# Optimization experiments

Measured on AMD Instinct MI355X. Metric: run time of the kernel, lower is better.

## Reference

```python
import jax, jax.numpy as jnp
import numpy as np

B, N, M, G, F = 8, 1000, 64, 50, 128


def setup_inputs() -> dict:
    key = jax.random.key(0)
    ks = jax.random.split(key, 9)
    s = 0.05
    return {
        "features": jax.random.normal(ks[0], (B, N, F), jnp.float32),
        "rbf_expansion": jax.random.uniform(ks[1], (B, N, M, G), jnp.float32),
        "neighbor_list": jax.random.randint(ks[2], (B, N, M), 0, N, jnp.int64),
        "W_init": jax.random.normal(ks[3], (F, F), jnp.float32) * s,
        "W1": jax.random.normal(ks[4], (G, F), jnp.float32) * s,
        "b1": jnp.zeros((F,), jnp.float32),
        "W2": jax.random.normal(ks[5], (F, F), jnp.float32) * s,
        "b2": jnp.zeros((F,), jnp.float32),
        "nbr_w": jax.random.normal(ks[6], (F,), jnp.float32) * s,
        "Wo1": jax.random.normal(ks[7], (F, F), jnp.float32) * s,
        "bo1": jnp.zeros((F,), jnp.float32),
        "Wo2": jax.random.normal(ks[8], (F, F), jnp.float32) * s,
        "bo2": jnp.zeros((F,), jnp.float32),
    }


def reference(features, rbf_expansion, neighbor_list, W_init, W1, b1, W2, b2,
              nbr_w, Wo1, bo1, Wo2, bo2):
    b, n, m = neighbor_list.shape
    # 1. atom-wise linear, no bias/activation: [B,N,F]
    init = features @ W_init
    # 2. CFConv: filter generator on RBF expansion -> [B,N,M,F]
    filt = jnp.tanh(rbf_expansion @ W1 + b1) @ W2 + b2
    # gather neighbor features: init[b, neighbor_list[b,n,m], :] -> [B,N,M,F]
    idx = neighbor_list.reshape(b, n * m, 1)
    nbr_feat = jnp.take_along_axis(init, idx, axis=1).reshape(b, n, m, -1)
    conv = nbr_feat * filt
    # attention over neighbors via learned vector nbr_w
    attn = jax.nn.softmax(jnp.einsum('bnmf,f->bnm', conv, nbr_w), axis=-1)
    agg = jnp.einsum('bnm,bnmf->bnf', attn, conv)
    # 3-4. output dense: linear+tanh, then linear
    out = jnp.tanh(agg @ Wo1 + bo1) @ Wo2 + bo2
    return out, attn
```

## Files before the change

kernel.cpp:

```cpp
#include <hip/hip_runtime.h>
#include <hip/hip_bf16.h>

typedef __attribute__((ext_vector_type(8))) short short8;
typedef __attribute__((ext_vector_type(4))) float f32x4;
typedef unsigned short u16;
typedef unsigned int u32;

#define NBATCH 8
#define NA 1000
#define MD 64
#define GD 50
#define FD 128
#define TOTAL (NBATCH * NA)

__device__ __forceinline__ u16 f2bf(float f) {
    u32 x = __float_as_uint(f);
    return (u16)((x + 0x7fffu + ((x >> 16) & 1u)) >> 16);
}
__device__ __forceinline__ float bf2f(u16 u) {
    return __uint_as_float(((u32)u) << 16);
}
__device__ __forceinline__ u32 pkbf(float x, float y) {
    __hip_bfloat162 h = __float22bfloat162_rn(float2{x, y});
    return *reinterpret_cast<u32*>(&h);
}
__device__ __forceinline__ float tanh_fast(float x) {
    float e = __expf(2.0f * x);
    return 1.0f - 2.0f * __builtin_amdgcn_rcpf(e + 1.0f);
}
__device__ __forceinline__ f32x4 mfma16(short8 a, short8 b, f32x4 c) {
    return __builtin_amdgcn_mfma_f32_16x16x32_bf16(a, b, c, 0, 0, 0);
}

__global__ void k0_prep(const float* __restrict__ W1, const float* __restrict__ W2,
                        const float* __restrict__ Wi, const float* __restrict__ Wo1,
                        const float* __restrict__ Wo2,
                        u16* __restrict__ W1P, u16* __restrict__ W2P,
                        u16* __restrict__ WiP, u16* __restrict__ Wo1P,
                        u16* __restrict__ Wo2P) {
    const int g0 = blockIdx.x * 256 + threadIdx.x;
    const int gstep = gridDim.x * 256;
    for (int p = g0; p < 16 * 512; p += gstep) {
        int seg = p >> 9, l = (p >> 3) & 63, j = p & 7;
        int ks = seg >> 3, nt = seg & 7;
        int k = ks * 32 + ((l >> 4) << 3) + j;
        int n = nt * 16 + (l & 15);
        W1P[p] = (k < GD) ? f2bf(W1[k * FD + n]) : (u16)0;
    }
    for (int p = g0; p < 32 * 512; p += gstep) {
        int seg = p >> 9, l = (p >> 3) & 63, j = p & 7;
        int half = seg >> 4, ks = (seg >> 3) & 1, nt = seg & 7;
        int k = half * 64 + ks * 32 + ((l >> 4) << 3) + j;
        int n = nt * 16 + (l & 15);
        int idx = k * FD + n;
        W2P[p]  = f2bf(W2[idx]);
        WiP[p]  = f2bf(Wi[idx]);
        Wo1P[p] = f2bf(Wo1[idx]);
        Wo2P[p] = f2bf(Wo2[idx]);
    }
}

__global__ __launch_bounds__(64) void k1_init(const float* __restrict__ feat,
                                              const u16* __restrict__ WiP,
                                              u16* __restrict__ initB) {
    const int lane = threadIdx.x;
    const int quad = lane >> 4, col = lane & 15;
    const int row0 = blockIdx.x * 16;

    f32x4 acc[8];
    const f32x4 zf = {0.f, 0.f, 0.f, 0.f};
#pragma unroll
    for (int nt = 0; nt < 8; ++nt) acc[nt] = zf;

#pragma unroll
    for (int half = 0; half < 2; ++half)
#pragma unroll
        for (int ks = 0; ks < 2; ++ks) {
            const int ka = half * 64 + ks * 32 + quad * 8;
            const float* src = &feat[(size_t)(row0 + col) * FD + ka];
            float4 v0 = *(const float4*)src;
            float4 v1 = *(const float4*)(src + 4);
            short8 a;
            u32* ap = (u32*)&a;
            ap[0] = pkbf(v0.x, v0.y);
            ap[1] = pkbf(v0.z, v0.w);
            ap[2] = pkbf(v1.x, v1.y);
            ap[3] = pkbf(v1.z, v1.w);
#pragma unroll
            for (int nt = 0; nt < 8; ++nt) {
                short8 bfr = *(const short8*)&WiP[(((half * 2 + ks) * 8 + nt) << 9) + (lane << 3)];
                acc[nt] = mfma16(a, bfr, acc[nt]);
            }
        }
#pragma unroll
    for (int nt = 0; nt < 8; ++nt)
#pragma unroll
        for (int r = 0; r < 4; ++r)
            initB[(size_t)(row0 + quad * 4 + r) * FD + nt * 16 + col] = f2bf(acc[nt][r]);
}

__global__ __launch_bounds__(256, 4) void k2_main(
    const float* __restrict__ rbf, const int* __restrict__ nl,
    const u16* __restrict__ initB,
    const u16* __restrict__ W1P, const u16* __restrict__ W2P,
    const float* __restrict__ b1, const float* __restrict__ b2,
    const float* __restrict__ nbrw,
    float* __restrict__ aggOut, float* __restrict__ attnO) {
    __shared__ alignas(16) char smem[34816];
    const int tid = threadIdx.x, wid = tid >> 6, lane = tid & 63;
    const int quad = lane >> 4, col = lane & 15, rw = wid * 32;
    const int blk = blockIdx.x;
    const int b = blk / 500;
    const int n0 = (blk - b * 500) * 2;
    const int atom0 = b * NA + n0;

    u16* wv = (u16*)smem + wid * 4352;
    float* logitS = (float*)smem;
    float* aggS   = (float*)(smem + 1024);

    int rowoff[2][4];
#pragma unroll
    for (int mt = 0; mt < 2; ++mt)
#pragma unroll
        for (int r = 0; r < 4; ++r)
            rowoff[mt][r] = (b * NA + nl[atom0 * MD + rw + mt * 16 + quad * 4 + r]) * FD;

    {
        const float* rsrc = rbf + (size_t)(atom0 * MD + rw) * GD;
        for (int i = lane; i < 800; i += 64) {
            int e = 2 * i;
            int r = e / 50, g = e - r * 50;
            float2 v = *(const float2*)&rsrc[e];
            *(u32*)&wv[r * 68 + g] = pkbf(v.x, v.y);
        }
        for (int i = lane; i < 448; i += 64) {
            int r = i / 14;
            wv[r * 68 + 50 + (i - r * 14)] = 0;
        }
    }

    f32x4 acc[2][8];
    const f32x4 zf = {0.f, 0.f, 0.f, 0.f};
#pragma unroll
    for (int mt = 0; mt < 2; ++mt)
#pragma unroll
        for (int nt = 0; nt < 8; ++nt) acc[mt][nt] = zf;
#pragma unroll
    for (int ks = 0; ks < 2; ++ks) {
        const int ka = ks * 32 + quad * 8;
        short8 a0 = *(const short8*)&wv[col * 68 + ka];
        short8 a1 = *(const short8*)&wv[(16 + col) * 68 + ka];
#pragma unroll
        for (int nt = 0; nt < 8; ++nt) {
            short8 bfr = *(const short8*)&W1P[((ks * 8 + nt) << 9) + (lane << 3)];
            acc[0][nt] = mfma16(a0, bfr, acc[0][nt]);
            acc[1][nt] = mfma16(a1, bfr, acc[1][nt]);
        }
    }

    float bias[8];
#pragma unroll
    for (int nt = 0; nt < 8; ++nt) bias[nt] = b1[nt * 16 + col];
#pragma unroll
    for (int mt = 0; mt < 2; ++mt)
#pragma unroll
        for (int nt = 0; nt < 8; ++nt)
#pragma unroll
            for (int r = 0; r < 4; ++r) {
                int row = mt * 16 + quad * 4 + r;
                wv[row * 136 + nt * 16 + col] =
                    f2bf(tanh_fast(acc[mt][nt][r] + bias[nt]));
            }

    f32x4 acc2[2][8];
#pragma unroll
    for (int mt = 0; mt < 2; ++mt)
#pragma unroll
        for (int nt = 0; nt < 8; ++nt) acc2[mt][nt] = zf;
#pragma unroll
    for (int half = 0; half < 2; ++half)
#pragma unroll
        for (int ks = 0; ks < 2; ++ks) {
            const int ka = half * 64 + ks * 32 + quad * 8;
            short8 a0 = *(const short8*)&wv[col * 136 + ka];
            short8 a1 = *(const short8*)&wv[(16 + col) * 136 + ka];
#pragma unroll
            for (int nt = 0; nt < 8; ++nt) {
                short8 bfr = *(const short8*)&W2P[(((half * 2 + ks) * 8 + nt) << 9) + (lane << 3)];
                acc2[0][nt] = mfma16(a0, bfr, acc2[0][nt]);
                acc2[1][nt] = mfma16(a1, bfr, acc2[1][nt]);
            }
        }

    float wv8[8];
#pragma unroll
    for (int nt = 0; nt < 8; ++nt) {
        bias[nt] = b2[nt * 16 + col];
        wv8[nt] = nbrw[nt * 16 + col];
    }
    float part[2][4] = {{0.f, 0.f, 0.f, 0.f}, {0.f, 0.f, 0.f, 0.f}};
#pragma unroll
    for (int mt = 0; mt < 2; ++mt)
#pragma unroll
        for (int nt = 0; nt < 8; ++nt)
#pragma unroll
            for (int r = 0; r < 4; ++r) {
                float nb = bf2f(initB[rowoff[mt][r] + nt * 16 + col]);
                float cv = nb * (acc2[mt][nt][r] + bias[nt]);
                acc2[mt][nt][r] = cv;
                part[mt][r] += cv * wv8[nt];
            }
#pragma unroll
    for (int d = 1; d < 16; d <<= 1)
#pragma unroll
        for (int mt = 0; mt < 2; ++mt)
#pragma unroll
            for (int r = 0; r < 4; ++r)
                part[mt][r] += __shfl_xor(part[mt][r], d, 64);

    __syncthreads();
    if (col == 0) {
#pragma unroll
        for (int mt = 0; mt < 2; ++mt)
#pragma unroll
            for (int r = 0; r < 4; ++r)
                logitS[rw + mt * 16 + quad * 4 + r] = part[mt][r];
    }
    __syncthreads();

    float attw[2][4];
    {
        const int base = rw & 64;
        float x = logitS[base + lane];
        float m = x;
#pragma unroll
        for (int d = 1; d < 64; d <<= 1) m = fmaxf(m, __shfl_xor(m, d, 64));
        float e = __expf(x - m);
        float s = e;
#pragma unroll
        for (int d = 1; d < 64; d <<= 1) s += __shfl_xor(s, d, 64);
        float a = e / s;
        if ((wid & 1) == 0)
            attnO[(size_t)(atom0 + (wid >> 1)) * MD + lane] = a;
#pragma unroll
        for (int mt = 0; mt < 2; ++mt)
#pragma unroll
            for (int r = 0; r < 4; ++r)
                attw[mt][r] = __shfl(a, (rw & 32) + mt * 16 + quad * 4 + r, 64);
    }

    float aggp[8] = {0.f, 0.f, 0.f, 0.f, 0.f, 0.f, 0.f, 0.f};
#pragma unroll
    for (int mt = 0; mt < 2; ++mt)
#pragma unroll
        for (int r = 0; r < 4; ++r) {
            float a = attw[mt][r];
#pragma unroll
            for (int nt = 0; nt < 8; ++nt) aggp[nt] += a * acc2[mt][nt][r];
        }
#pragma unroll
    for (int d = 16; d < 64; d <<= 1)
#pragma unroll
        for (int nt = 0; nt < 8; ++nt) aggp[nt] += __shfl_xor(aggp[nt], d, 64);
    if (quad == 0) {
#pragma unroll
        for (int nt = 0; nt < 8; ++nt) aggS[wid * 128 + nt * 16 + col] = aggp[nt];
    }
    __syncthreads();
    {
        int a = tid >> 7;
        int c = tid & 127;
        float v = aggS[(2 * a) * 128 + c] + aggS[(2 * a + 1) * 128 + c];
        aggOut[(size_t)(atom0 + a) * FD + c] = v;
    }
}

__global__ __launch_bounds__(64) void k3_out(
    float* __restrict__ outp, const u16* __restrict__ Wo1P,
    const u16* __restrict__ Wo2P, const float* __restrict__ bo1,
    const float* __restrict__ bo2) {
    __shared__ alignas(16) u16 sT[16 * 136];
    const int lane = threadIdx.x;
    const int quad = lane >> 4, col = lane & 15;
    const int row0 = blockIdx.x * 16;

    f32x4 acc[8];
    const f32x4 zf = {0.f, 0.f, 0.f, 0.f};
#pragma unroll
    for (int nt = 0; nt < 8; ++nt) acc[nt] = zf;
#pragma unroll
    for (int half = 0; half < 2; ++half)
#pragma unroll
        for (int ks = 0; ks < 2; ++ks) {
            const int ka = half * 64 + ks * 32 + quad * 8;
            const float* src = &outp[(size_t)(row0 + col) * FD + ka];
            float4 v0 = *(const float4*)src;
            float4 v1 = *(const float4*)(src + 4);
            short8 a;
            u32* ap = (u32*)&a;
            ap[0] = pkbf(v0.x, v0.y);
            ap[1] = pkbf(v0.z, v0.w);
            ap[2] = pkbf(v1.x, v1.y);
            ap[3] = pkbf(v1.z, v1.w);
#pragma unroll
            for (int nt = 0; nt < 8; ++nt) {
                short8 bfr = *(const short8*)&Wo1P[(((half * 2 + ks) * 8 + nt) << 9) + (lane << 3)];
                acc[nt] = mfma16(a, bfr, acc[nt]);
            }
        }

#pragma unroll
    for (int nt = 0; nt < 8; ++nt) {
        float bias = bo1[nt * 16 + col];
#pragma unroll
        for (int r = 0; r < 4; ++r)
            sT[(quad * 4 + r) * 136 + nt * 16 + col] =
                f2bf(tanh_fast(acc[nt][r] + bias));
    }
    __syncthreads();

    f32x4 acc2[8];
#pragma unroll
    for (int nt = 0; nt < 8; ++nt) acc2[nt] = zf;
#pragma unroll
    for (int half = 0; half < 2; ++half)
#pragma unroll
        for (int ks = 0; ks < 2; ++ks) {
            const int ka = half * 64 + ks * 32 + quad * 8;
            short8 a0 = *(const short8*)&sT[col * 136 + ka];
#pragma unroll
            for (int nt = 0; nt < 8; ++nt) {
                short8 bfr = *(const short8*)&Wo2P[(((half * 2 + ks) * 8 + nt) << 9) + (lane << 3)];
                acc2[nt] = mfma16(a0, bfr, acc2[nt]);
            }
        }
#pragma unroll
    for (int nt = 0; nt < 8; ++nt) {
        float bias = bo2[nt * 16 + col];
#pragma unroll
        for (int r = 0; r < 4; ++r)
            outp[(size_t)(row0 + quad * 4 + r) * FD + nt * 16 + col] =
                acc2[nt][r] + bias;
    }
}

extern "C" void kernel_launch(void* const* d_in, const int* in_sizes, int n_in,
                              void* d_out, int out_size, void* d_ws,
                              size_t ws_size, hipStream_t stream) {
    const float* feat = (const float*)d_in[0];
    const float* rbf  = (const float*)d_in[1];
    const int*   nl   = (const int*)d_in[2];
    const float* Wi   = (const float*)d_in[3];
    const float* W1   = (const float*)d_in[4];
    const float* b1   = (const float*)d_in[5];
    const float* W2   = (const float*)d_in[6];
    const float* b2   = (const float*)d_in[7];
    const float* nbrw = (const float*)d_in[8];
    const float* Wo1  = (const float*)d_in[9];
    const float* bo1  = (const float*)d_in[10];
    const float* Wo2  = (const float*)d_in[11];
    const float* bo2  = (const float*)d_in[12];

    float* outp  = (float*)d_out;
    float* attnp = outp + (size_t)TOTAL * FD;

    char* ws = (char*)d_ws;
    u16* initB = (u16*)ws;
    u16* W1P   = (u16*)(ws + 2048000);
    u16* W2P   = (u16*)(ws + 2064384);
    u16* WiP   = (u16*)(ws + 2097152);
    u16* Wo1P  = (u16*)(ws + 2129920);
    u16* Wo2P  = (u16*)(ws + 2162688);

    hipLaunchKernelGGL(k0_prep, dim3(40), dim3(256), 0, stream,
                       W1, W2, Wi, Wo1, Wo2, W1P, W2P, WiP, Wo1P, Wo2P);
    hipLaunchKernelGGL(k1_init, dim3(500), dim3(64), 0, stream, feat, WiP, initB);
    hipLaunchKernelGGL(k2_main, dim3(4000), dim3(256), 0, stream,
                       rbf, nl, initB, W1P, W2P, b1, b2, nbrw, outp, attnp);
    hipLaunchKernelGGL(k3_out, dim3(500), dim3(64), 0, stream,
                       outp, Wo1P, Wo2P, bo1, bo2);
}
```

Baseline: 261.2 us.

## Fuse four kernels into one persistent cooperative kernel with grid syncs

Replaces the four separate launches (weight prep, init linear, main CFConv/attention, output MLP) with one cooperative persistent kernel. The phases are separated by grid-wide syncs, and blocks loop over work items in a grid-stride fashion. This removes the launch and inter-kernel gaps. In exchange it adds three grid barriers, and the small phases now run with fewer, larger blocks (a wave per 16-row tile), which may reduce parallelism compared with 500 separate blocks.

```diff
diff --git a/kernel.cpp b/kernel.cpp
--- a/kernel.cpp
+++ b/kernel.cpp
@@ -1,5 +1,8 @@
 #include <hip/hip_runtime.h>
 #include <hip/hip_bf16.h>
+#include <hip/hip_cooperative_groups.h>
+
+namespace cg = cooperative_groups;
 
 typedef __attribute__((ext_vector_type(8))) short short8;
 typedef __attribute__((ext_vector_type(4))) float f32x4;
@@ -32,14 +35,25 @@
     return __builtin_amdgcn_mfma_f32_16x16x32_bf16(a, b, c, 0, 0, 0);
 }
 
-__global__ void k0_prep(const float* __restrict__ W1, const float* __restrict__ W2,
-                        const float* __restrict__ Wi, const float* __restrict__ Wo1,
-                        const float* __restrict__ Wo2,
-                        u16* __restrict__ W1P, u16* __restrict__ W2P,
-                        u16* __restrict__ WiP, u16* __restrict__ Wo1P,
-                        u16* __restrict__ Wo2P) {
-    const int g0 = blockIdx.x * 256 + threadIdx.x;
-    const int gstep = gridDim.x * 256;
+__global__ __launch_bounds__(256, 4) void fused(
+    const float* __restrict__ feat, const float* __restrict__ rbf,
+    const int* __restrict__ nl,
+    const float* __restrict__ Wi, const float* __restrict__ W1,
+    const float* __restrict__ b1, const float* __restrict__ W2,
+    const float* __restrict__ b2, const float* __restrict__ nbrw,
+    const float* __restrict__ Wo1, const float* __restrict__ bo1,
+    const float* __restrict__ Wo2, const float* __restrict__ bo2,
+    u16* __restrict__ initB, u16* __restrict__ W1P, u16* __restrict__ W2P,
+    u16* __restrict__ WiP, u16* __restrict__ Wo1P, u16* __restrict__ Wo2P,
+    float* __restrict__ outp, float* __restrict__ attnp) {
+    cg::grid_group grid = cg::this_grid();
+    __shared__ alignas(16) char smem[34816];
+    const int tid = threadIdx.x, wid = tid >> 6, lane = tid & 63;
+    const int quad = lane >> 4, col = lane & 15, rw = wid * 32;
+    const int nblk = gridDim.x, blk = blockIdx.x;
+    const int g0 = blk * 256 + tid, gstep = nblk * 256;
+    const f32x4 zf = {0.f, 0.f, 0.f, 0.f};
+
     for (int p = g0; p < 16 * 512; p += gstep) {
         int seg = p >> 9, l = (p >> 3) & 63, j = p & 7;
         int ks = seg >> 3, nt = seg & 7;
@@ -58,289 +72,272 @@
         Wo1P[p] = f2bf(Wo1[idx]);
         Wo2P[p] = f2bf(Wo2[idx]);
     }
-}
-
-__global__ __launch_bounds__(64) void k1_init(const float* __restrict__ feat,
-                                              const u16* __restrict__ WiP,
-                                              u16* __restrict__ initB) {
-    const int lane = threadIdx.x;
-    const int quad = lane >> 4, col = lane & 15;
-    const int row0 = blockIdx.x * 16;
-
-    f32x4 acc[8];
-    const f32x4 zf = {0.f, 0.f, 0.f, 0.f};
-#pragma unroll
-    for (int nt = 0; nt < 8; ++nt) acc[nt] = zf;
-
-#pragma unroll
-    for (int half = 0; half < 2; ++half)
-#pragma unroll
-        for (int ks = 0; ks < 2; ++ks) {
-            const int ka = half * 64 + ks * 32 + quad * 8;
-            const float* src = &feat[(size_t)(row0 + col) * FD + ka];
-            float4 v0 = *(const float4*)src;
-            float4 v1 = *(const float4*)(src + 4);
-            short8 a;
-            u32* ap = (u32*)&a;
-            ap[0] = pkbf(v0.x, v0.y);
-            ap[1] = pkbf(v0.z, v0.w);
-            ap[2] = pkbf(v1.x, v1.y);
-            ap[3] = pkbf(v1.z, v1.w);
-#pragma unroll
-            for (int nt = 0; nt < 8; ++nt) {
-                short8 bfr = *(const short8*)&WiP[(((half * 2 + ks) * 8 + nt) << 9) + (lane << 3)];
-                acc[nt] = mfma16(a, bfr, acc[nt]);
-            }
+    __threadfence();
+    grid.sync();
+
+    for (int t = blk * 4 + wid; t < 500; t += nblk * 4) {
+        const int row0 = t * 16;
+        f32x4 acc[8];
+#pragma unroll
+        for (int nt = 0; nt < 8; ++nt) acc[nt] = zf;
+#pragma unroll
+        for (int half = 0; half < 2; ++half)
+#pragma unroll
+            for (int ks = 0; ks < 2; ++ks) {
+                const int ka = half * 64 + ks * 32 + quad * 8;
+                const float* src = &feat[(size_t)(row0 + col) * FD + ka];
+                float4 v0 = *(const float4*)src;
+                float4 v1 = *(const float4*)(src + 4);
+                short8 a;
+                u32* ap = (u32*)&a;
+                ap[0] = pkbf(v0.x, v0.y);
+                ap[1] = pkbf(v0.z, v0.w);
+                ap[2] = pkbf(v1.x, v1.y);
+                ap[3] = pkbf(v1.z, v1.w);
+#pragma unroll
+                for (int nt = 0; nt < 8; ++nt) {
+                    short8 bfr = *(const short8*)&WiP[(((half * 2 + ks) * 8 + nt) << 9) + (lane << 3)];
+                    acc[nt] = mfma16(a, bfr, acc[nt]);
+                }
+            }
+#pragma unroll
+        for (int nt = 0; nt < 8; ++nt)
+#pragma unroll
+            for (int r = 0; r < 4; ++r)
+                initB[(size_t)(row0 + quad * 4 + r) * FD + nt * 16 + col] = f2bf(acc[nt][r]);
+    }
+    __threadfence();
+    grid.sync();
+
+    {
+        u16* wv = (u16*)smem + wid * 4352;
+        float* logitS = (float*)smem;
+        float* aggS   = (float*)(smem + 1024);
+
+        float b1v[8], b2v[8], wvv[8];
+#pragma unroll
+        for (int nt = 0; nt < 8; ++nt) {
+            b1v[nt] = b1[nt * 16 + col];
+            b2v[nt] = b2[nt * 16 + col];
+            wvv[nt] = nbrw[nt * 16 + col];
         }
-#pragma unroll
-    for (int nt = 0; nt < 8; ++nt)
-#pragma unroll
-        for (int r = 0; r < 4; ++r)
-            initB[(size_t)(row0 + quad * 4 + r) * FD + nt * 16 + col] = f2bf(acc[nt][r]);
-}
-
-__global__ __launch_bounds__(256, 4) void k2_main(
-    const float* __restrict__ rbf, const int* __restrict__ nl,
-    const u16* __restrict__ initB,
-    const u16* __restrict__ W1P, const u16* __restrict__ W2P,
-    const float* __restrict__ b1, const float* __restrict__ b2,
-    const float* __restrict__ nbrw,
-    float* __restrict__ aggOut, float* __restrict__ attnO) {
-    __shared__ alignas(16) char smem[34816];
-    const int tid = threadIdx.x, wid = tid >> 6, lane = tid & 63;
-    const int quad = lane >> 4, col = lane & 15, rw = wid * 32;
-    const int blk = blockIdx.x;
-    const int b = blk / 500;
-    const int n0 = (blk - b * 500) * 2;
-    const int atom0 = b * NA + n0;
-
-    u16* wv = (u16*)smem + wid * 4352;
-    float* logitS = (float*)smem;
-    float* aggS   = (float*)(smem + 1024);
-
-    int rowoff[2][4];
-#pragma unroll
-    for (int mt = 0; mt < 2; ++mt)
-#pragma unroll
-        for (int r = 0; r < 4; ++r)
-            rowoff[mt][r] = (b * NA + nl[atom0 * MD + rw + mt * 16 + quad * 4 + r]) * FD;
-
-    {
-        const float* rsrc = rbf + (size_t)(atom0 * MD + rw) * GD;
-        for (int i = lane; i < 800; i += 64) {
-            int e = 2 * i;
-            int r = e / 50, g = e - r * 50;
-            float2 v = *(const float2*)&rsrc[e];
-            *(u32*)&wv[r * 68 + g] = pkbf(v.x, v.y);
+
+        for (int pair = blk; pair < 4000; pair += nblk) {
+            const int b = pair / 500;
+            const int n0 = (pair - b * 500) * 2;
+            const int atom0 = b * NA + n0;
+
+            int rowoff[2][4];
+#pragma unroll
+            for (int mt = 0; mt < 2; ++mt)
+#pragma unroll
+                for (int r = 0; r < 4; ++r)
+                    rowoff[mt][r] = (b * NA + nl[atom0 * MD + rw + mt * 16 + quad * 4 + r]) * FD;
+
+            {
+                const float* rsrc = rbf + (size_t)(atom0 * MD + rw) * GD;
+                for (int i = lane; i < 800; i += 64) {
+                    int e = 2 * i;
+                    int r = e / 50, g = e - r * 50;
+                    float2 v = *(const float2*)&rsrc[e];
+                    *(u32*)&wv[r * 68 + g] = pkbf(v.x, v.y);
+                }
+                for (int i = lane; i < 448; i += 64) {
+                    int r = i / 14;
+                    wv[r * 68 + 50 + (i - r * 14)] = 0;
+                }
+            }
+
+            f32x4 acc[2][8];
+#pragma unroll
+            for (int mt = 0; mt < 2; ++mt)
+#pragma unroll
+                for (int nt = 0; nt < 8; ++nt) acc[mt][nt] = zf;
+#pragma unroll
+            for (int ks = 0; ks < 2; ++ks) {
+                const int ka = ks * 32 + quad * 8;
+                short8 a0 = *(const short8*)&wv[col * 68 + ka];
+                short8 a1 = *(const short8*)&wv[(16 + col) * 68 + ka];
+#pragma unroll
+                for (int nt = 0; nt < 8; ++nt) {
+                    short8 bfr = *(const short8*)&W1P[((ks * 8 + nt) << 9) + (lane << 3)];
+                    acc[0][nt] = mfma16(a0, bfr, acc[0][nt]);
+                    acc[1][nt] = mfma16(a1, bfr, acc[1][nt]);
+                }
+            }
+
+#pragma unroll
+            for (int mt = 0; mt < 2; ++mt)
+#pragma unroll
+                for (int nt = 0; nt < 8; ++nt)
+#pragma unroll
+                    for (int r = 0; r < 4; ++r) {
+                        int row = mt * 16 + quad * 4 + r;
+                        wv[row * 136 + nt * 16 + col] =
+                            f2bf(tanh_fast(acc[mt][nt][r] + b1v[nt]));
+                    }
+
+            f32x4 acc2[2][8];
+#pragma unroll
+            for (int mt = 0; mt < 2; ++mt)
+#pragma unroll
+                for (int nt = 0; nt < 8; ++nt) acc2[mt][nt] = zf;
+#pragma unroll
+            for (int half = 0; half < 2; ++half)
+#pragma unroll
+                for (int ks = 0; ks < 2; ++ks) {
+                    const int ka = half * 64 + ks * 32 + quad * 8;
+                    short8 a0 = *(const short8*)&wv[col * 136 + ka];
+                    short8 a1 = *(const short8*)&wv[(16 + col) * 136 + ka];
+#pragma unroll
+                    for (int nt = 0; nt < 8; ++nt) {
+                        short8 bfr = *(const short8*)&W2P[(((half * 2 + ks) * 8 + nt) << 9) + (lane << 3)];
+                        acc2[0][nt] = mfma16(a0, bfr, acc2[0][nt]);
+                        acc2[1][nt] = mfma16(a1, bfr, acc2[1][nt]);
+                    }
+                }
+
+            float part[2][4] = {{0.f, 0.f, 0.f, 0.f}, {0.f, 0.f, 0.f, 0.f}};
+#pragma unroll
+            for (int mt = 0; mt < 2; ++mt)
+#pragma unroll
+                for (int nt = 0; nt < 8; ++nt)
+#pragma unroll
+                    for (int r = 0; r < 4; ++r) {
+                        float nb = bf2f(initB[rowoff[mt][r] + nt * 16 + col]);
+                        float cv = nb * (acc2[mt][nt][r] + b2v[nt]);
+                        acc2[mt][nt][r] = cv;
+                        part[mt][r] += cv * wvv[nt];
+                    }
+#pragma unroll
+            for (int d = 1; d < 16; d <<= 1)
+#pragma unroll
+                for (int mt = 0; mt < 2; ++mt)
+#pragma unroll
+                    for (int r = 0; r < 4; ++r)
+                        part[mt][r] += __shfl_xor(part[mt][r], d, 64);
+
+            __syncthreads();
+            if (col == 0) {
+#pragma unroll
+                for (int mt = 0; mt < 2; ++mt)
+#pragma unroll
+                    for (int r = 0; r < 4; ++r)
+                        logitS[rw + mt * 16 + quad * 4 + r] = part[mt][r];
+            }
+            __syncthreads();
+
+            float attw[2][4];
+            {
+                const int base = rw & 64;
+                float x = logitS[base + lane];
+                float m = x;
+#pragma unroll
+                for (int d = 1; d < 64; d <<= 1) m = fmaxf(m, __shfl_xor(m, d, 64));
+                float e = __expf(x - m);
+                float s = e;
+#pragma unroll
+                for (int d = 1; d < 64; d <<= 1) s += __shfl_xor(s, d, 64);
+                float a = e / s;
+                if ((wid & 1) == 0)
+                    attnp[(size_t)(atom0 + (wid >> 1)) * MD + lane] = a;
+#pragma unroll
+                for (int mt = 0; mt < 2; ++mt)
+#pragma unroll
+                    for (int r = 0; r < 4; ++r)
+                        attw[mt][r] = __shfl(a, (rw & 32) + mt * 16 + quad * 4 + r, 64);
+            }
+
+            float aggp[8] = {0.f, 0.f, 0.f, 0.f, 0.f, 0.f, 0.f, 0.f};
+#pragma unroll
+            for (int mt = 0; mt < 2; ++mt)
+#pragma unroll
+                for (int r = 0; r < 4; ++r) {
+                    float a = attw[mt][r];
+#pragma unroll
+                    for (int nt = 0; nt < 8; ++nt) aggp[nt] += a * acc2[mt][nt][r];
+                }
+#pragma unroll
+            for (int d = 16; d < 64; d <<= 1)
+#pragma unroll
+                for (int nt = 0; nt < 8; ++nt) aggp[nt] += __shfl_xor(aggp[nt], d, 64);
+            if (quad == 0) {
+#pragma unroll
+                for (int nt = 0; nt < 8; ++nt) aggS[wid * 128 + nt * 16 + col] = aggp[nt];
+            }
+            __syncthreads();
+            {
+                int a = tid >> 7;
+                int c = tid & 127;
+                float v = aggS[(2 * a) * 128 + c] + aggS[(2 * a + 1) * 128 + c];
+                outp[(size_t)(atom0 + a) * FD + c] = v;
+            }
+            __syncthreads();
         }
-        for (int i = lane; i < 448; i += 64) {
-            int r = i / 14;
-            wv[r * 68 + 50 + (i - r * 14)] = 0;
+    }
+    __threadfence();
+    grid.sync();
+
+    for (int t = blk * 4 + wid; t < 500; t += nblk * 4) {
+        const int row0 = t * 16;
+        u16* sT = (u16*)(smem + wid * 8704);
+
+        f32x4 acc[8];
+#pragma unroll
+        for (int nt = 0; nt < 8; ++nt) acc[nt] = zf;
+#pragma unroll
+        for (int half = 0; half < 2; ++half)
+#pragma unroll
+            for (int ks = 0; ks < 2; ++ks) {
+                const int ka = half * 64 + ks * 32 + quad * 8;
+                const float* src = &outp[(size_t)(row0 + col) * FD + ka];
+                float4 v0 = *(const float4*)src;
+                float4 v1 = *(const float4*)(src + 4);
+                short8 a;
+                u32* ap = (u32*)&a;
+                ap[0] = pkbf(v0.x, v0.y);
+                ap[1] = pkbf(v0.z, v0.w);
+                ap[2] = pkbf(v1.x, v1.y);
+                ap[3] = pkbf(v1.z, v1.w);
+#pragma unroll
+                for (int nt = 0; nt < 8; ++nt) {
+                    short8 bfr = *(const short8*)&Wo1P[(((half * 2 + ks) * 8 + nt) << 9) + (lane << 3)];
+                    acc[nt] = mfma16(a, bfr, acc[nt]);
+                }
+            }
+
+#pragma unroll
+        for (int nt = 0; nt < 8; ++nt) {
+            float bias = bo1[nt * 16 + col];
+#pragma unroll
+            for (int r = 0; r < 4; ++r)
+                sT[(quad * 4 + r) * 136 + nt * 16 + col] =
+                    f2bf(tanh_fast(acc[nt][r] + bias));
         }
-    }
-
-    f32x4 acc[2][8];
-    const f32x4 zf = {0.f, 0.f, 0.f, 0.f};
-#pragma unroll
-    for (int mt = 0; mt < 2; ++mt)
-#pragma unroll
-        for (int nt = 0; nt < 8; ++nt) acc[mt][nt] = zf;
-#pragma unroll
-    for (int ks = 0; ks < 2; ++ks) {
-        const int ka = ks * 32 + quad * 8;
-        short8 a0 = *(const short8*)&wv[col * 68 + ka];
-        short8 a1 = *(const short8*)&wv[(16 + col) * 68 + ka];
+
+        f32x4 acc2[8];
+#pragma unroll
+        for (int nt = 0; nt < 8; ++nt) acc2[nt] = zf;
+#pragma unroll
+        for (int half = 0; half < 2; ++half)
+#pragma unroll
+            for (int ks = 0; ks < 2; ++ks) {
+                const int ka = half * 64 + ks * 32 + quad * 8;
+                short8 a0 = *(const short8*)&sT[col * 136 + ka];
+#pragma unroll
+                for (int nt = 0; nt < 8; ++nt) {
+                    short8 bfr = *(const short8*)&Wo2P[(((half * 2 + ks) * 8 + nt) << 9) + (lane << 3)];
+                    acc2[nt] = mfma16(a0, bfr, acc2[nt]);
+                }
+            }
 #pragma unroll
         for (int nt = 0; nt < 8; ++nt) {
-            short8 bfr = *(const short8*)&W1P[((ks * 8 + nt) << 9) + (lane << 3)];
-            acc[0][nt] = mfma16(a0, bfr, acc[0][nt]);
-            acc[1][nt] = mfma16(a1, bfr, acc[1][nt]);
+            float bias = bo2[nt * 16 + col];
+#pragma unroll
+            for (int r = 0; r < 4; ++r)
+                outp[(size_t)(row0 + quad * 4 + r) * FD + nt * 16 + col] =
+                    acc2[nt][r] + bias;
         }
-    }
-
-    float bias[8];
-#pragma unroll
-    for (int nt = 0; nt < 8; ++nt) bias[nt] = b1[nt * 16 + col];
-#pragma unroll
-    for (int mt = 0; mt < 2; ++mt)
-#pragma unroll
-        for (int nt = 0; nt < 8; ++nt)
-#pragma unroll
-            for (int r = 0; r < 4; ++r) {
-                int row = mt * 16 + quad * 4 + r;
-                wv[row * 136 + nt * 16 + col] =
-                    f2bf(tanh_fast(acc[mt][nt][r] + bias[nt]));
-            }
-
-    f32x4 acc2[2][8];
-#pragma unroll
-    for (int mt = 0; mt < 2; ++mt)
-#pragma unroll
-        for (int nt = 0; nt < 8; ++nt) acc2[mt][nt] = zf;
-#pragma unroll
-    for (int half = 0; half < 2; ++half)
-#pragma unroll
-        for (int ks = 0; ks < 2; ++ks) {
-            const int ka = half * 64 + ks * 32 + quad * 8;
-            short8 a0 = *(const short8*)&wv[col * 136 + ka];
-            short8 a1 = *(const short8*)&wv[(16 + col) * 136 + ka];
-#pragma unroll
-            for (int nt = 0; nt < 8; ++nt) {
-                short8 bfr = *(const short8*)&W2P[(((half * 2 + ks) * 8 + nt) << 9) + (lane << 3)];
-                acc2[0][nt] = mfma16(a0, bfr, acc2[0][nt]);
-                acc2[1][nt] = mfma16(a1, bfr, acc2[1][nt]);
-            }
-        }
-
-    float wv8[8];
-#pragma unroll
-    for (int nt = 0; nt < 8; ++nt) {
-        bias[nt] = b2[nt * 16 + col];
-        wv8[nt] = nbrw[nt * 16 + col];
-    }
-    float part[2][4] = {{0.f, 0.f, 0.f, 0.f}, {0.f, 0.f, 0.f, 0.f}};
-#pragma unroll
-    for (int mt = 0; mt < 2; ++mt)
-#pragma unroll
-        for (int nt = 0; nt < 8; ++nt)
-#pragma unroll
-            for (int r = 0; r < 4; ++r) {
-                float nb = bf2f(initB[rowoff[mt][r] + nt * 16 + col]);
-                float cv = nb * (acc2[mt][nt][r] + bias[nt]);
-                acc2[mt][nt][r] = cv;
-                part[mt][r] += cv * wv8[nt];
-            }
-#pragma unroll
-    for (int d = 1; d < 16; d <<= 1)
-#pragma unroll
-        for (int mt = 0; mt < 2; ++mt)
-#pragma unroll
-            for (int r = 0; r < 4; ++r)
-                part[mt][r] += __shfl_xor(part[mt][r], d, 64);
-
-    __syncthreads();
-    if (col == 0) {
-#pragma unroll
-        for (int mt = 0; mt < 2; ++mt)
-#pragma unroll
-            for (int r = 0; r < 4; ++r)
-                logitS[rw + mt * 16 + quad * 4 + r] = part[mt][r];
-    }
-    __syncthreads();
-
-    float attw[2][4];
-    {
-        const int base = rw & 64;
-        float x = logitS[base + lane];
-        float m = x;
-#pragma unroll
-        for (int d = 1; d < 64; d <<= 1) m = fmaxf(m, __shfl_xor(m, d, 64));
-        float e = __expf(x - m);
-        float s = e;
-#pragma unroll
-        for (int d = 1; d < 64; d <<= 1) s += __shfl_xor(s, d, 64);
-        float a = e / s;
-        if ((wid & 1) == 0)
-            attnO[(size_t)(atom0 + (wid >> 1)) * MD + lane] = a;
-#pragma unroll
-        for (int mt = 0; mt < 2; ++mt)
-#pragma unroll
-            for (int r = 0; r < 4; ++r)
-                attw[mt][r] = __shfl(a, (rw & 32) + mt * 16 + quad * 4 + r, 64);
-    }
-
-    float aggp[8] = {0.f, 0.f, 0.f, 0.f, 0.f, 0.f, 0.f, 0.f};
-#pragma unroll
-    for (int mt = 0; mt < 2; ++mt)
-#pragma unroll
-        for (int r = 0; r < 4; ++r) {
-            float a = attw[mt][r];
-#pragma unroll
-            for (int nt = 0; nt < 8; ++nt) aggp[nt] += a * acc2[mt][nt][r];
-        }
-#pragma unroll
-    for (int d = 16; d < 64; d <<= 1)
-#pragma unroll
-        for (int nt = 0; nt < 8; ++nt) aggp[nt] += __shfl_xor(aggp[nt], d, 64);
-    if (quad == 0) {
-#pragma unroll
-        for (int nt = 0; nt < 8; ++nt) aggS[wid * 128 + nt * 16 + col] = aggp[nt];
-    }
-    __syncthreads();
-    {
-        int a = tid >> 7;
-        int c = tid & 127;
-        float v = aggS[(2 * a) * 128 + c] + aggS[(2 * a + 1) * 128 + c];
-        aggOut[(size_t)(atom0 + a) * FD + c] = v;
-    }
-}
-
-__global__ __launch_bounds__(64) void k3_out(
-    float* __restrict__ outp, const u16* __restrict__ Wo1P,
-    const u16* __restrict__ Wo2P, const float* __restrict__ bo1,
-    const float* __restrict__ bo2) {
-    __shared__ alignas(16) u16 sT[16 * 136];
-    const int lane = threadIdx.x;
-    const int quad = lane >> 4, col = lane & 15;
-    const int row0 = blockIdx.x * 16;
-
-    f32x4 acc[8];
-    const f32x4 zf = {0.f, 0.f, 0.f, 0.f};
-#pragma unroll
-    for (int nt = 0; nt < 8; ++nt) acc[nt] = zf;
-#pragma unroll
-    for (int half = 0; half < 2; ++half)
-#pragma unroll
-        for (int ks = 0; ks < 2; ++ks) {
-            const int ka = half * 64 + ks * 32 + quad * 8;
-            const float* src = &outp[(size_t)(row0 + col) * FD + ka];
-            float4 v0 = *(const float4*)src;
-            float4 v1 = *(const float4*)(src + 4);
-            short8 a;
-            u32* ap = (u32*)&a;
-            ap[0] = pkbf(v0.x, v0.y);
-            ap[1] = pkbf(v0.z, v0.w);
-            ap[2] = pkbf(v1.x, v1.y);
-            ap[3] = pkbf(v1.z, v1.w);
-#pragma unroll
-            for (int nt = 0; nt < 8; ++nt) {
-                short8 bfr = *(const short8*)&Wo1P[(((half * 2 + ks) * 8 + nt) << 9) + (lane << 3)];
-                acc[nt] = mfma16(a, bfr, acc[nt]);
-            }
-        }
-
-#pragma unroll
-    for (int nt = 0; nt < 8; ++nt) {
-        float bias = bo1[nt * 16 + col];
-#pragma unroll
-        for (int r = 0; r < 4; ++r)
-            sT[(quad * 4 + r) * 136 + nt * 16 + col] =
-                f2bf(tanh_fast(acc[nt][r] + bias));
-    }
-    __syncthreads();
-
-    f32x4 acc2[8];
-#pragma unroll
-    for (int nt = 0; nt < 8; ++nt) acc2[nt] = zf;
-#pragma unroll
-    for (int half = 0; half < 2; ++half)
-#pragma unroll
-        for (int ks = 0; ks < 2; ++ks) {
-            const int ka = half * 64 + ks * 32 + quad * 8;
-            short8 a0 = *(const short8*)&sT[col * 136 + ka];
-#pragma unroll
-            for (int nt = 0; nt < 8; ++nt) {
-                short8 bfr = *(const short8*)&Wo2P[(((half * 2 + ks) * 8 + nt) << 9) + (lane << 3)];
-                acc2[nt] = mfma16(a0, bfr, acc2[nt]);
-            }
-        }
-#pragma unroll
-    for (int nt = 0; nt < 8; ++nt) {
-        float bias = bo2[nt * 16 + col];
-#pragma unroll
-        for (int r = 0; r < 4; ++r)
-            outp[(size_t)(row0 + quad * 4 + r) * FD + nt * 16 + col] =
-                acc2[nt][r] + bias;
     }
 }
 
@@ -372,11 +369,23 @@
     u16* Wo1P  = (u16*)(ws + 2129920);
     u16* Wo2P  = (u16*)(ws + 2162688);
 
-    hipLaunchKernelGGL(k0_prep, dim3(40), dim3(256), 0, stream,
-                       W1, W2, Wi, Wo1, Wo2, W1P, W2P, WiP, Wo1P, Wo2P);
-    hipLaunchKernelGGL(k1_init, dim3(500), dim3(64), 0, stream, feat, WiP, initB);
-    hipLaunchKernelGGL(k2_main, dim3(4000), dim3(256), 0, stream,
-                       rbf, nl, initB, W1P, W2P, b1, b2, nbrw, outp, attnp);
-    hipLaunchKernelGGL(k3_out, dim3(500), dim3(64), 0, stream,
-                       outp, Wo1P, Wo2P, bo1, bo2);
-}
+    static int nblk = 0;
+    if (nblk == 0) {
+        int dev = 0;
+        hipGetDevice(&dev);
+        hipDeviceProp_t props;
+        hipGetDeviceProperties(&props, dev);
+        int mbp = 0;
+        hipOccupancyMaxActiveBlocksPerMultiprocessor(&mbp, (const void*)fused, 256, 0);
+        if (mbp < 1) mbp = 1;
+        if (mbp > 4) mbp = 4;
+        nblk = props.multiProcessorCount * mbp;
+        if (nblk > 4000) nblk = 4000;
+        if (nblk < 64) nblk = 64;
+    }
+
+    void* args[] = {&feat, &rbf, &nl, &Wi, &W1, &b1, &W2, &b2, &nbrw,
+                    &Wo1, &bo1, &Wo2, &bo2,
+                    &initB, &W1P, &W2P, &WiP, &Wo1P, &Wo2P, &outp, &attnp};
+    hipLaunchCooperativeKernel((const void*)fused, dim3(nblk), dim3(256), args, 0, stream);
+}
```

Result: slower. 847.1 us (+224.3%).

## Interleave init feature layout for vector gathers and fuse output MLP into main kernel

Applied to the files above, without the earlier changes.

Stores the bf16 init features in an interleaved column order so each neighbor row gather in the main kernel becomes one 16-byte load per lane instead of eight scalar loads. Also fuses the output dense layers into the main kernel, computing the two-atom output MLP with MFMA from shared memory, which removes a separate launch and the global round trip of the aggregated features. The fused MLP uses MFMA tiles that are mostly padding and adds extra barriers per block.

```diff
diff --git a/kernel.cpp b/kernel.cpp
--- a/kernel.cpp
+++ b/kernel.cpp
@@ -93,10 +93,12 @@
             }
         }
 #pragma unroll
-    for (int nt = 0; nt < 8; ++nt)
-#pragma unroll
-        for (int r = 0; r < 4; ++r)
-            initB[(size_t)(row0 + quad * 4 + r) * FD + nt * 16 + col] = f2bf(acc[nt][r]);
+    for (int r = 0; r < 4; ++r) {
+        short8 g;
+#pragma unroll
+        for (int nt = 0; nt < 8; ++nt) g[nt] = (short)f2bf(acc[nt][r]);
+        *(short8*)&initB[(size_t)(row0 + quad * 4 + r) * FD + col * 8] = g;
+    }
 }
 
 __global__ __launch_bounds__(256, 4) void k2_main(
@@ -105,7 +107,9 @@
     const u16* __restrict__ W1P, const u16* __restrict__ W2P,
     const float* __restrict__ b1, const float* __restrict__ b2,
     const float* __restrict__ nbrw,
-    float* __restrict__ aggOut, float* __restrict__ attnO) {
+    const u16* __restrict__ Wo1P, const u16* __restrict__ Wo2P,
+    const float* __restrict__ bo1, const float* __restrict__ bo2,
+    float* __restrict__ outp, float* __restrict__ attnO) {
     __shared__ alignas(16) char smem[34816];
     const int tid = threadIdx.x, wid = tid >> 6, lane = tid & 63;
     const int quad = lane >> 4, col = lane & 15, rw = wid * 32;
@@ -117,6 +121,8 @@
     u16* wv = (u16*)smem + wid * 4352;
     float* logitS = (float*)smem;
     float* aggS   = (float*)(smem + 1024);
+    u16* aggF = (u16*)(smem + 4096);
+    u16* t1F  = (u16*)(smem + 8704 + 4352);
 
     int rowoff[2][4];
 #pragma unroll
@@ -202,14 +208,16 @@
 #pragma unroll
     for (int mt = 0; mt < 2; ++mt)
 #pragma unroll
-        for (int nt = 0; nt < 8; ++nt)
-#pragma unroll
-            for (int r = 0; r < 4; ++r) {
-                float nb = bf2f(initB[rowoff[mt][r] + nt * 16 + col]);
+        for (int r = 0; r < 4; ++r) {
+            short8 g = *(const short8*)&initB[rowoff[mt][r] + col * 8];
+#pragma unroll
+            for (int nt = 0; nt < 8; ++nt) {
+                float nb = bf2f((u16)g[nt]);
                 float cv = nb * (acc2[mt][nt][r] + bias[nt]);
                 acc2[mt][nt][r] = cv;
                 part[mt][r] += cv * wv8[nt];
             }
+        }
 #pragma unroll
     for (int d = 1; d < 16; d <<= 1)
 #pragma unroll
@@ -267,80 +275,57 @@
         for (int nt = 0; nt < 8; ++nt) aggS[wid * 128 + nt * 16 + col] = aggp[nt];
     }
     __syncthreads();
+
     {
-        int a = tid >> 7;
-        int c = tid & 127;
+        int a = tid >> 7, c = tid & 127;
         float v = aggS[(2 * a) * 128 + c] + aggS[(2 * a + 1) * 128 + c];
-        aggOut[(size_t)(atom0 + a) * FD + c] = v;
-    }
-}
-
-__global__ __launch_bounds__(64) void k3_out(
-    float* __restrict__ outp, const u16* __restrict__ Wo1P,
-    const u16* __restrict__ Wo2P, const float* __restrict__ bo1,
-    const float* __restrict__ bo2) {
-    __shared__ alignas(16) u16 sT[16 * 136];
-    const int lane = threadIdx.x;
-    const int quad = lane >> 4, col = lane & 15;
-    const int row0 = blockIdx.x * 16;
-
-    f32x4 acc[8];
-    const f32x4 zf = {0.f, 0.f, 0.f, 0.f};
-#pragma unroll
-    for (int nt = 0; nt < 8; ++nt) acc[nt] = zf;
+        aggF[a * 136 + c] = f2bf(v);
+    }
+    __syncthreads();
+
+    f32x4 o0 = zf, o1v = zf;
 #pragma unroll
     for (int half = 0; half < 2; ++half)
 #pragma unroll
         for (int ks = 0; ks < 2; ++ks) {
             const int ka = half * 64 + ks * 32 + quad * 8;
-            const float* src = &outp[(size_t)(row0 + col) * FD + ka];
-            float4 v0 = *(const float4*)src;
-            float4 v1 = *(const float4*)(src + 4);
-            short8 a;
-            u32* ap = (u32*)&a;
-            ap[0] = pkbf(v0.x, v0.y);
-            ap[1] = pkbf(v0.z, v0.w);
-            ap[2] = pkbf(v1.x, v1.y);
-            ap[3] = pkbf(v1.z, v1.w);
-#pragma unroll
-            for (int nt = 0; nt < 8; ++nt) {
-                short8 bfr = *(const short8*)&Wo1P[(((half * 2 + ks) * 8 + nt) << 9) + (lane << 3)];
-                acc[nt] = mfma16(a, bfr, acc[nt]);
-            }
-        }
-
-#pragma unroll
-    for (int nt = 0; nt < 8; ++nt) {
-        float bias = bo1[nt * 16 + col];
-#pragma unroll
-        for (int r = 0; r < 4; ++r)
-            sT[(quad * 4 + r) * 136 + nt * 16 + col] =
-                f2bf(tanh_fast(acc[nt][r] + bias));
-    }
-    __syncthreads();
-
-    f32x4 acc2[8];
-#pragma unroll
-    for (int nt = 0; nt < 8; ++nt) acc2[nt] = zf;
+            short8 a0 = *(const short8*)&aggF[col * 136 + ka];
+            short8 bf0 = *(const short8*)&Wo1P[(((half * 2 + ks) * 8 + 2 * wid) << 9) + (lane << 3)];
+            short8 bf1 = *(const short8*)&Wo1P[(((half * 2 + ks) * 8 + 2 * wid + 1) << 9) + (lane << 3)];
+            o0 = mfma16(a0, bf0, o0);
+            o1v = mfma16(a0, bf1, o1v);
+        }
+    if (quad == 0) {
+        float bb0 = bo1[(2 * wid) * 16 + col];
+        float bb1 = bo1[(2 * wid + 1) * 16 + col];
+#pragma unroll
+        for (int r = 0; r < 2; ++r) {
+            t1F[r * 136 + (2 * wid) * 16 + col] = f2bf(tanh_fast(o0[r] + bb0));
+            t1F[r * 136 + (2 * wid + 1) * 16 + col] = f2bf(tanh_fast(o1v[r] + bb1));
+        }
+    }
+    __syncthreads();
+
+    o0 = zf; o1v = zf;
 #pragma unroll
     for (int half = 0; half < 2; ++half)
 #pragma unroll
         for (int ks = 0; ks < 2; ++ks) {
             const int ka = half * 64 + ks * 32 + quad * 8;
-            short8 a0 = *(const short8*)&sT[col * 136 + ka];
-#pragma unroll
-            for (int nt = 0; nt < 8; ++nt) {
-                short8 bfr = *(const short8*)&Wo2P[(((half * 2 + ks) * 8 + nt) << 9) + (lane << 3)];
-                acc2[nt] = mfma16(a0, bfr, acc2[nt]);
-            }
-        }
-#pragma unroll
-    for (int nt = 0; nt < 8; ++nt) {
-        float bias = bo2[nt * 16 + col];
-#pragma unroll
-        for (int r = 0; r < 4; ++r)
-            outp[(size_t)(row0 + quad * 4 + r) * FD + nt * 16 + col] =
-                acc2[nt][r] + bias;
+            short8 a0 = *(const short8*)&t1F[col * 136 + ka];
+            short8 bf0 = *(const short8*)&Wo2P[(((half * 2 + ks) * 8 + 2 * wid) << 9) + (lane << 3)];
+            short8 bf1 = *(const short8*)&Wo2P[(((half * 2 + ks) * 8 + 2 * wid + 1) << 9) + (lane << 3)];
+            o0 = mfma16(a0, bf0, o0);
+            o1v = mfma16(a0, bf1, o1v);
+        }
+    if (quad == 0) {
+        float bb0 = bo2[(2 * wid) * 16 + col];
+        float bb1 = bo2[(2 * wid + 1) * 16 + col];
+#pragma unroll
+        for (int r = 0; r < 2; ++r) {
+            outp[(size_t)(atom0 + r) * FD + (2 * wid) * 16 + col] = o0[r] + bb0;
+            outp[(size_t)(atom0 + r) * FD + (2 * wid + 1) * 16 + col] = o1v[r] + bb1;
+        }
     }
 }
 
@@ -376,7 +361,6 @@
                        W1, W2, Wi, Wo1, Wo2, W1P, W2P, WiP, Wo1P, Wo2P);
     hipLaunchKernelGGL(k1_init, dim3(500), dim3(64), 0, stream, feat, WiP, initB);
     hipLaunchKernelGGL(k2_main, dim3(4000), dim3(256), 0, stream,
-                       rbf, nl, initB, W1P, W2P, b1, b2, nbrw, outp, attnp);
-    hipLaunchKernelGGL(k3_out, dim3(500), dim3(64), 0, stream,
-                       outp, Wo1P, Wo2P, bo1, bo2);
-}
+                       rbf, nl, initB, W1P, W2P, b1, b2, nbrw,
+                       Wo1P, Wo2P, bo1, bo2, outp, attnp);
+}
```

Measured after the change: 268.1 us. +2.6%, slower.

## Permute feature layout for vectorized bf16 stores and gathers; fold biases into accumulators

Applied to the files above, without the earlier changes.

Stores the init features and intermediate tanh activations in a column-permuted order, so each lane writes and reads one 16-byte short8 instead of eight scattered 2-byte elements. W2 and Wo2 get matching K-permuted packing so the GEMMs still compute the right result. The main win sought is vectorising the random neighbor gather from initB in k2. Biases are also preloaded into the MFMA accumulators, which removes the separate add. This adds coupling between the prep permutation and the consumer kernels, so any mismatch would silently corrupt results.

```diff
diff --git a/kernel.cpp b/kernel.cpp
--- a/kernel.cpp
+++ b/kernel.cpp
@@ -50,13 +50,13 @@
     for (int p = g0; p < 32 * 512; p += gstep) {
         int seg = p >> 9, l = (p >> 3) & 63, j = p & 7;
         int half = seg >> 4, ks = (seg >> 3) & 1, nt = seg & 7;
-        int k = half * 64 + ks * 32 + ((l >> 4) << 3) + j;
+        int kstor = half * 64 + ks * 32 + ((l >> 4) << 3) + j;
         int n = nt * 16 + (l & 15);
-        int idx = k * FD + n;
-        W2P[p]  = f2bf(W2[idx]);
-        WiP[p]  = f2bf(Wi[idx]);
-        Wo1P[p] = f2bf(Wo1[idx]);
-        Wo2P[p] = f2bf(Wo2[idx]);
+        WiP[p]  = f2bf(Wi[kstor * FD + n]);
+        Wo1P[p] = f2bf(Wo1[kstor * FD + n]);
+        int kperm = (kstor >> 3) | ((kstor & 7) << 4);
+        W2P[p]  = f2bf(W2[kperm * FD + n]);
+        Wo2P[p] = f2bf(Wo2[kperm * FD + n]);
     }
 }
 
@@ -93,10 +93,15 @@
             }
         }
 #pragma unroll
-    for (int nt = 0; nt < 8; ++nt)
-#pragma unroll
-        for (int r = 0; r < 4; ++r)
-            initB[(size_t)(row0 + quad * 4 + r) * FD + nt * 16 + col] = f2bf(acc[nt][r]);
+    for (int r = 0; r < 4; ++r) {
+        short8 g;
+        u32* gp = (u32*)&g;
+        gp[0] = pkbf(acc[0][r], acc[1][r]);
+        gp[1] = pkbf(acc[2][r], acc[3][r]);
+        gp[2] = pkbf(acc[4][r], acc[5][r]);
+        gp[3] = pkbf(acc[6][r], acc[7][r]);
+        *(short8*)&initB[(size_t)(row0 + quad * 4 + r) * FD + col * 8] = g;
+    }
 }
 
 __global__ __launch_bounds__(256, 4) void k2_main(
@@ -140,11 +145,13 @@
     }
 
     f32x4 acc[2][8];
-    const f32x4 zf = {0.f, 0.f, 0.f, 0.f};
-#pragma unroll
-    for (int mt = 0; mt < 2; ++mt)
-#pragma unroll
-        for (int nt = 0; nt < 8; ++nt) acc[mt][nt] = zf;
+#pragma unroll
+    for (int nt = 0; nt < 8; ++nt) {
+        float bb = b1[nt * 16 + col];
+        f32x4 c = {bb, bb, bb, bb};
+        acc[0][nt] = c;
+        acc[1][nt] = c;
+    }
 #pragma unroll
     for (int ks = 0; ks < 2; ++ks) {
         const int ka = ks * 32 + quad * 8;
@@ -158,25 +165,27 @@
         }
     }
 
-    float bias[8];
-#pragma unroll
-    for (int nt = 0; nt < 8; ++nt) bias[nt] = b1[nt * 16 + col];
 #pragma unroll
     for (int mt = 0; mt < 2; ++mt)
 #pragma unroll
-        for (int nt = 0; nt < 8; ++nt)
-#pragma unroll
-            for (int r = 0; r < 4; ++r) {
-                int row = mt * 16 + quad * 4 + r;
-                wv[row * 136 + nt * 16 + col] =
-                    f2bf(tanh_fast(acc[mt][nt][r] + bias[nt]));
-            }
+        for (int r = 0; r < 4; ++r) {
+            short8 h;
+            u32* hp = (u32*)&h;
+            hp[0] = pkbf(tanh_fast(acc[mt][0][r]), tanh_fast(acc[mt][1][r]));
+            hp[1] = pkbf(tanh_fast(acc[mt][2][r]), tanh_fast(acc[mt][3][r]));
+            hp[2] = pkbf(tanh_fast(acc[mt][4][r]), tanh_fast(acc[mt][5][r]));
+            hp[3] = pkbf(tanh_fast(acc[mt][6][r]), tanh_fast(acc[mt][7][r]));
+            *(short8*)&wv[(mt * 16 + quad * 4 + r) * 136 + col * 8] = h;
+        }
 
     f32x4 acc2[2][8];
 #pragma unroll
-    for (int mt = 0; mt < 2; ++mt)
-#pragma unroll
-        for (int nt = 0; nt < 8; ++nt) acc2[mt][nt] = zf;
+    for (int nt = 0; nt < 8; ++nt) {
+        float bb = b2[nt * 16 + col];
+        f32x4 c = {bb, bb, bb, bb};
+        acc2[0][nt] = c;
+        acc2[1][nt] = c;
+    }
 #pragma unroll
     for (int half = 0; half < 2; ++half)
 #pragma unroll
@@ -194,22 +203,21 @@
 
     float wv8[8];
 #pragma unroll
-    for (int nt = 0; nt < 8; ++nt) {
-        bias[nt] = b2[nt * 16 + col];
-        wv8[nt] = nbrw[nt * 16 + col];
-    }
+    for (int nt = 0; nt < 8; ++nt) wv8[nt] = nbrw[nt * 16 + col];
     float part[2][4] = {{0.f, 0.f, 0.f, 0.f}, {0.f, 0.f, 0.f, 0.f}};
 #pragma unroll
     for (int mt = 0; mt < 2; ++mt)
 #pragma unroll
-        for (int nt = 0; nt < 8; ++nt)
-#pragma unroll
-            for (int r = 0; r < 4; ++r) {
-                float nb = bf2f(initB[rowoff[mt][r] + nt * 16 + col]);
-                float cv = nb * (acc2[mt][nt][r] + bias[nt]);
+        for (int r = 0; r < 4; ++r) {
+            short8 g = *(const short8*)&initB[rowoff[mt][r] + col * 8];
+#pragma unroll
+            for (int nt = 0; nt < 8; ++nt) {
+                float nb = bf2f((u16)g[nt]);
+                float cv = nb * acc2[mt][nt][r];
                 acc2[mt][nt][r] = cv;
                 part[mt][r] += cv * wv8[nt];
             }
+        }
 #pragma unroll
     for (int d = 1; d < 16; d <<= 1)
 #pragma unroll
@@ -285,9 +293,12 @@
     const int row0 = blockIdx.x * 16;
 
     f32x4 acc[8];
-    const f32x4 zf = {0.f, 0.f, 0.f, 0.f};
-#pragma unroll
-    for (int nt = 0; nt < 8; ++nt) acc[nt] = zf;
+#pragma unroll
+    for (int nt = 0; nt < 8; ++nt) {
+        float bb = bo1[nt * 16 + col];
+        f32x4 c = {bb, bb, bb, bb};
+        acc[nt] = c;
+    }
 #pragma unroll
     for (int half = 0; half < 2; ++half)
 #pragma unroll
@@ -310,18 +321,24 @@
         }
 
 #pragma unroll
+    for (int r = 0; r < 4; ++r) {
+        short8 h;
+        u32* hp = (u32*)&h;
+        hp[0] = pkbf(tanh_fast(acc[0][r]), tanh_fast(acc[1][r]));
+        hp[1] = pkbf(tanh_fast(acc[2][r]), tanh_fast(acc[3][r]));
+        hp[2] = pkbf(tanh_fast(acc[4][r]), tanh_fast(acc[5][r]));
+        hp[3] = pkbf(tanh_fast(acc[6][r]), tanh_fast(acc[7][r]));
+        *(short8*)&sT[(quad * 4 + r) * 136 + col * 8] = h;
+    }
+    __syncthreads();
+
+    f32x4 acc2[8];
+#pragma unroll
     for (int nt = 0; nt < 8; ++nt) {
-        float bias = bo1[nt * 16 + col];
-#pragma unroll
-        for (int r = 0; r < 4; ++r)
-            sT[(quad * 4 + r) * 136 + nt * 16 + col] =
-                f2bf(tanh_fast(acc[nt][r] + bias));
-    }
-    __syncthreads();
-
-    f32x4 acc2[8];
-#pragma unroll
-    for (int nt = 0; nt < 8; ++nt) acc2[nt] = zf;
+        float bb = bo2[nt * 16 + col];
+        f32x4 c = {bb, bb, bb, bb};
+        acc2[nt] = c;
+    }
 #pragma unroll
     for (int half = 0; half < 2; ++half)
 #pragma unroll
@@ -335,13 +352,10 @@
             }
         }
 #pragma unroll
-    for (int nt = 0; nt < 8; ++nt) {
-        float bias = bo2[nt * 16 + col];
+    for (int nt = 0; nt < 8; ++nt)
 #pragma unroll
         for (int r = 0; r < 4; ++r)
-            outp[(size_t)(row0 + quad * 4 + r) * FD + nt * 16 + col] =
-                acc2[nt][r] + bias;
-    }
+            outp[(size_t)(row0 + quad * 4 + r) * FD + nt * 16 + col] = acc2[nt][r];
 }
 
 extern "C" void kernel_launch(void* const* d_in, const int* in_sizes, int n_in,
```

Result: no change. 259.7 us (-0.6%).
